# Kernel tuning notes

Hardware: AMD Instinct MI355X
Metric: run time of the kernel (lower is better)

The kernel has to match this reference:

```python
import jax, jax.numpy as jnp
import numpy as np

N_NODES = 50000
N_EDGES = 800000
D = 64
N_LAYERS = 3  # layer_dims = [64, 64, 64, 64]


def setup_inputs() -> dict:
    key = jax.random.key(0)
    ks = jax.random.split(key, 5)
    x = jax.random.normal(ks[0], (N_NODES, D), dtype=jnp.float32)
    edge_index = jax.random.randint(ks[1], (2, N_EDGES), 0, N_NODES, dtype=jnp.int64)
    scale = 1.0 / np.sqrt(D)
    # Per-layer restriction (message) maps, self-loop maps, and biases.
    W_msg = jax.random.normal(ks[2], (N_LAYERS, D, D), dtype=jnp.float32) * scale
    W_self = jax.random.normal(ks[3], (N_LAYERS, D, D), dtype=jnp.float32) * scale
    b = jax.random.normal(ks[4], (N_LAYERS, D), dtype=jnp.float32) * 0.01
    return {"x": x, "edge_index": edge_index, "W_msg": W_msg, "W_self": W_self, "b": b}


def reference(x, edge_index, W_msg, W_self, b):
    """Stacked sheaf conv layers: per-edge gather -> linear restriction ->
    scatter-sum aggregation to destination nodes + self-loop linear + bias,
    with ReLU between layers (none after the final layer)."""
    n = x.shape[0]
    src, dst = edge_index[0], edge_index[1]
    n_layers = W_msg.shape[0]
    for i in range(n_layers):
        msg = x[src] @ W_msg[i]                                   # [E, d] gather + restriction
        agg = jax.ops.segment_sum(msg, dst, num_segments=n)       # [N, d] scatter-add
        x = x @ W_self[i] + agg + b[i]                            # self-loop + aggregate + bias
        if i < n_layers - 1:
            x = jax.nn.relu(x)
    return x
```

## Files before the change

kernel.cpp:

```cpp
#include <hip/hip_runtime.h>

#define D 64

__device__ __forceinline__ unsigned short f2bf(float f) {
    unsigned u = __float_as_uint(f);
    unsigned r = (u + 0x7FFFu + ((u >> 16) & 1u)) >> 16;
    return (unsigned short)r;
}
__device__ __forceinline__ float bf2f(unsigned short h) {
    return __uint_as_float((unsigned)h << 16);
}

typedef __attribute__((ext_vector_type(8))) short bf16x8;
typedef __attribute__((ext_vector_type(4))) float f32x4;

__global__ void prep_kernel(const float* __restrict__ x, unsigned short* __restrict__ xb,
                            int total, int* __restrict__ deg, int N,
                            const float* __restrict__ Wself,
                            const float* __restrict__ Wmsg,
                            unsigned short* __restrict__ Bt, int n_layers) {
    int i = blockIdx.x * blockDim.x + threadIdx.x;
    if (i < N) deg[i] = 0;
    int wtotal = n_layers * D * 2 * D;
    if (i < wtotal) {
        int k = i & 127;
        int n = (i >> 7) & 63;
        int l = i >> 13;
        float w = (k < D) ? Wself[(size_t)l * D * D + k * D + n]
                          : Wmsg [(size_t)l * D * D + (k - D) * D + n];
        unsigned short hi = f2bf(w);
        unsigned short lo = f2bf(w - bf2f(hi));
        size_t base = (size_t)l * 2 * D * 2 * D;
        Bt[base + (size_t)n * 128 + k] = hi;
        Bt[base + 8192 + (size_t)n * 128 + k] = lo;
    }
    int base = i * 4;
    if (base + 4 <= total) {
        float4 v = *reinterpret_cast<const float4*>(x + base);
        ushort4 o;
        o.x = f2bf(v.x); o.y = f2bf(v.y); o.z = f2bf(v.z); o.w = f2bf(v.w);
        *reinterpret_cast<ushort4*>(xb + base) = o;
    } else if (base < total) {
        for (int k = base; k < total; ++k) xb[k] = f2bf(x[k]);
    }
}

__global__ void hist_rank_kernel(const int* __restrict__ dst, int* __restrict__ deg,
                                 int* __restrict__ rank, int E) {
    int i = blockIdx.x * blockDim.x + threadIdx.x;
    int base = i * 8;
    if (base + 8 <= E) {
        int4 d0 = *reinterpret_cast<const int4*>(dst + base);
        int4 d1 = *reinterpret_cast<const int4*>(dst + base + 4);
        int4 r0, r1;
        r0.x = atomicAdd(&deg[d0.x], 1);
        r0.y = atomicAdd(&deg[d0.y], 1);
        r0.z = atomicAdd(&deg[d0.z], 1);
        r0.w = atomicAdd(&deg[d0.w], 1);
        r1.x = atomicAdd(&deg[d1.x], 1);
        r1.y = atomicAdd(&deg[d1.y], 1);
        r1.z = atomicAdd(&deg[d1.z], 1);
        r1.w = atomicAdd(&deg[d1.w], 1);
        *reinterpret_cast<int4*>(rank + base) = r0;
        *reinterpret_cast<int4*>(rank + base + 4) = r1;
    } else {
        for (int e = base; e < E; ++e) rank[e] = atomicAdd(&deg[dst[e]], 1);
    }
}

__global__ void scan_k1(const int* __restrict__ deg, int* __restrict__ bsum, int n) {
    __shared__ int sh[256];
    int t = threadIdx.x;
    int g = blockIdx.x * 256 + t;
    int v = (g < n) ? deg[g] : 0;
    sh[t] = v;
    __syncthreads();
    for (int off = 1; off < 256; off <<= 1) {
        int u = (t >= off) ? sh[t - off] : 0;
        __syncthreads();
        sh[t] += u;
        __syncthreads();
    }
    if (t == 255) bsum[blockIdx.x] = sh[255];
}

__global__ void scan_k2(const int* __restrict__ bsum, int* __restrict__ boff, int nb) {
    __shared__ int sh[1024];
    int t = threadIdx.x;
    int v = (t < nb) ? bsum[t] : 0;
    sh[t] = v;
    __syncthreads();
    for (int off = 1; off < 1024; off <<= 1) {
        int u = (t >= off) ? sh[t - off] : 0;
        __syncthreads();
        sh[t] += u;
        __syncthreads();
    }
    if (t < nb) boff[t] = sh[t] - v;
}

__global__ void scan_k3(const int* __restrict__ deg, const int* __restrict__ boff,
                        int* __restrict__ row_ptr, int n) {
    __shared__ int sh[256];
    int t = threadIdx.x;
    int g = blockIdx.x * 256 + t;
    int v = (g < n) ? deg[g] : 0;
    sh[t] = v;
    __syncthreads();
    for (int off = 1; off < 256; off <<= 1) {
        int u = (t >= off) ? sh[t - off] : 0;
        __syncthreads();
        sh[t] += u;
        __syncthreads();
    }
    if (g < n) {
        int excl = sh[t] - v + boff[blockIdx.x];
        row_ptr[g] = excl;
        if (g == n - 1) row_ptr[n] = excl + v;
    }
}

__global__ void perm_rank_kernel(const int* __restrict__ src, const int* __restrict__ dst,
                                 const int* __restrict__ rank, const int* __restrict__ row_ptr,
                                 int* __restrict__ sorted_src, int E) {
    int i = blockIdx.x * blockDim.x + threadIdx.x;
    int base = i * 8;
    if (base + 8 <= E) {
        int4 d0 = *reinterpret_cast<const int4*>(dst + base);
        int4 d1 = *reinterpret_cast<const int4*>(dst + base + 4);
        int4 s0 = *reinterpret_cast<const int4*>(src + base);
        int4 s1 = *reinterpret_cast<const int4*>(src + base + 4);
        int4 r0 = *reinterpret_cast<const int4*>(rank + base);
        int4 r1 = *reinterpret_cast<const int4*>(rank + base + 4);
        int p0 = row_ptr[d0.x] + r0.x;
        int p1 = row_ptr[d0.y] + r0.y;
        int p2 = row_ptr[d0.z] + r0.z;
        int p3 = row_ptr[d0.w] + r0.w;
        int p4 = row_ptr[d1.x] + r1.x;
        int p5 = row_ptr[d1.y] + r1.y;
        int p6 = row_ptr[d1.z] + r1.z;
        int p7 = row_ptr[d1.w] + r1.w;
        __builtin_nontemporal_store(s0.x, &sorted_src[p0]);
        __builtin_nontemporal_store(s0.y, &sorted_src[p1]);
        __builtin_nontemporal_store(s0.z, &sorted_src[p2]);
        __builtin_nontemporal_store(s0.w, &sorted_src[p3]);
        __builtin_nontemporal_store(s1.x, &sorted_src[p4]);
        __builtin_nontemporal_store(s1.y, &sorted_src[p5]);
        __builtin_nontemporal_store(s1.z, &sorted_src[p6]);
        __builtin_nontemporal_store(s1.w, &sorted_src[p7]);
    } else {
        for (int e = base; e < E; ++e)
            sorted_src[row_ptr[dst[e]] + rank[e]] = src[e];
    }
}

__device__ __forceinline__ void acc16(float* ac, uint4 u0, uint4 u1) {
    ac[0]  += __uint_as_float(u0.x << 16);
    ac[1]  += __uint_as_float(u0.x & 0xFFFF0000u);
    ac[2]  += __uint_as_float(u0.y << 16);
    ac[3]  += __uint_as_float(u0.y & 0xFFFF0000u);
    ac[4]  += __uint_as_float(u0.z << 16);
    ac[5]  += __uint_as_float(u0.z & 0xFFFF0000u);
    ac[6]  += __uint_as_float(u0.w << 16);
    ac[7]  += __uint_as_float(u0.w & 0xFFFF0000u);
    ac[8]  += __uint_as_float(u1.x << 16);
    ac[9]  += __uint_as_float(u1.x & 0xFFFF0000u);
    ac[10] += __uint_as_float(u1.y << 16);
    ac[11] += __uint_as_float(u1.y & 0xFFFF0000u);
    ac[12] += __uint_as_float(u1.z << 16);
    ac[13] += __uint_as_float(u1.z & 0xFFFF0000u);
    ac[14] += __uint_as_float(u1.w << 16);
    ac[15] += __uint_as_float(u1.w & 0xFFFF0000u);
}

__global__ void __launch_bounds__(256)
fused_layer(const unsigned short* __restrict__ xb,
            const int* __restrict__ row_ptr,
            const int* __restrict__ sorted_src,
            const unsigned short* __restrict__ Bt,
            const float* __restrict__ bias,
            float* __restrict__ out_f32,
            unsigned short* __restrict__ out_bf16,
            int n_nodes, int E, int last) {
    __shared__ float red[4][16][68];

    int lane = threadIdx.x & 63;
    int w    = threadIdx.x >> 6;
    int ln15 = lane & 15;
    int lhi  = lane >> 4;

    int node0 = blockIdx.x << 4;
    int node  = node0 + ln15;
    int ncl   = min(node, n_nodes - 1);
    int beg = row_ptr[ncl];
    int end = row_ptr[ncl + 1];
    if (node >= n_nodes) end = beg;
    int deg = end - beg;

    int md = deg;
    md = max(md, __shfl_xor(md, 1));
    md = max(md, __shfl_xor(md, 2));
    md = max(md, __shfl_xor(md, 4));
    md = max(md, __shfl_xor(md, 8));

    float ac[16];
#pragma unroll
    for (int t = 0; t < 16; ++t) ac[t] = 0.f;

    const int Em1 = E - 1;
    int p = w;
    for (; p + 4 < md; p += 8) {
        int cA = min(beg + p,     Em1);
        int cB = min(beg + p + 4, Em1);
        int sA = sorted_src[cA];
        int sB = sorted_src[cB];
        const unsigned short* rA = xb + (((size_t)(unsigned)sA) << 6) + (lhi << 3);
        const unsigned short* rB = xb + (((size_t)(unsigned)sB) << 6) + (lhi << 3);
        uint4 a0 = *reinterpret_cast<const uint4*>(rA);
        uint4 a1 = *reinterpret_cast<const uint4*>(rA + 32);
        uint4 b0 = *reinterpret_cast<const uint4*>(rB);
        uint4 b1 = *reinterpret_cast<const uint4*>(rB + 32);
        if (p < deg)     acc16(ac, a0, a1);
        if (p + 4 < deg) acc16(ac, b0, b1);
    }
    for (; p < md; p += 4) {
        int cA = min(beg + p, Em1);
        int sA = sorted_src[cA];
        const unsigned short* rA = xb + (((size_t)(unsigned)sA) << 6) + (lhi << 3);
        uint4 a0 = *reinterpret_cast<const uint4*>(rA);
        uint4 a1 = *reinterpret_cast<const uint4*>(rA + 32);
        if (p < deg) acc16(ac, a0, a1);
    }

    int f0 = lhi << 3;
    *reinterpret_cast<float4*>(&red[w][ln15][f0])      = make_float4(ac[0], ac[1], ac[2], ac[3]);
    *reinterpret_cast<float4*>(&red[w][ln15][f0 + 4])  = make_float4(ac[4], ac[5], ac[6], ac[7]);
    *reinterpret_cast<float4*>(&red[w][ln15][32 + f0]) = make_float4(ac[8], ac[9], ac[10], ac[11]);
    *reinterpret_cast<float4*>(&red[w][ln15][36 + f0]) = make_float4(ac[12], ac[13], ac[14], ac[15]);

    bf16x8 Bf[2][4];
    {
        const unsigned short* bp = Bt + ((size_t)(w * 16 + ln15)) * 128 + (lhi << 3);
#pragma unroll
        for (int pp = 0; pp < 2; ++pp)
#pragma unroll
            for (int kc = 0; kc < 4; ++kc)
                Bf[pp][kc] = *reinterpret_cast<const bf16x8*>(bp + pp * 8192 + kc * 32);
    }
    const unsigned short* xr = xb + (((size_t)(unsigned)ncl) << 6) + (lhi << 3);
    bf16x8 A0 = *reinterpret_cast<const bf16x8*>(xr);
    bf16x8 A1 = *reinterpret_cast<const bf16x8*>(xr + 32);
    float bb = bias[w * 16 + ln15];

    __syncthreads();

    float s[16];
#pragma unroll
    for (int t = 0; t < 16; ++t) s[t] = 0.f;
#pragma unroll
    for (int ww = 0; ww < 4; ++ww) {
        float4 r0 = *reinterpret_cast<const float4*>(&red[ww][ln15][f0]);
        float4 r1 = *reinterpret_cast<const float4*>(&red[ww][ln15][f0 + 4]);
        float4 r2 = *reinterpret_cast<const float4*>(&red[ww][ln15][32 + f0]);
        float4 r3 = *reinterpret_cast<const float4*>(&red[ww][ln15][36 + f0]);
        s[0]  += r0.x; s[1]  += r0.y; s[2]  += r0.z; s[3]  += r0.w;
        s[4]  += r1.x; s[5]  += r1.y; s[6]  += r1.z; s[7]  += r1.w;
        s[8]  += r2.x; s[9]  += r2.y; s[10] += r2.z; s[11] += r2.w;
        s[12] += r3.x; s[13] += r3.y; s[14] += r3.z; s[15] += r3.w;
    }
    bf16x8 A2, A3;
#pragma unroll
    for (int t = 0; t < 8; ++t) A2[t] = (short)f2bf(s[t]);
#pragma unroll
    for (int t = 0; t < 8; ++t) A3[t] = (short)f2bf(s[8 + t]);

    f32x4 c = {0.f, 0.f, 0.f, 0.f};
    c = __builtin_amdgcn_mfma_f32_16x16x32_bf16(A0, Bf[0][0], c, 0, 0, 0);
    c = __builtin_amdgcn_mfma_f32_16x16x32_bf16(A0, Bf[1][0], c, 0, 0, 0);
    c = __builtin_amdgcn_mfma_f32_16x16x32_bf16(A1, Bf[0][1], c, 0, 0, 0);
    c = __builtin_amdgcn_mfma_f32_16x16x32_bf16(A1, Bf[1][1], c, 0, 0, 0);
    c = __builtin_amdgcn_mfma_f32_16x16x32_bf16(A2, Bf[0][2], c, 0, 0, 0);
    c = __builtin_amdgcn_mfma_f32_16x16x32_bf16(A2, Bf[1][2], c, 0, 0, 0);
    c = __builtin_amdgcn_mfma_f32_16x16x32_bf16(A3, Bf[0][3], c, 0, 0, 0);
    c = __builtin_amdgcn_mfma_f32_16x16x32_bf16(A3, Bf[1][3], c, 0, 0, 0);

    int colo = w * 16 + ln15;
    if (last) {
#pragma unroll
        for (int r = 0; r < 4; ++r) {
            int nr = node0 + lhi * 4 + r;
            if (nr < n_nodes)
                out_f32[((size_t)(unsigned)nr << 6) + colo] = c[r] + bb;
        }
    } else {
#pragma unroll
        for (int r = 0; r < 4; ++r) {
            int nr = node0 + lhi * 4 + r;
            if (nr < n_nodes)
                out_bf16[((size_t)(unsigned)nr << 6) + colo] = f2bf(fmaxf(c[r] + bb, 0.f));
        }
    }
}

__global__ void scatter_kernel(const float* __restrict__ x,
                               const int* __restrict__ src,
                               const int* __restrict__ dst,
                               float* __restrict__ agg, int n_edges) {
    int e = blockIdx.x * (blockDim.x >> 6) + (threadIdx.x >> 6);
    int lane = threadIdx.x & 63;
    if (e >= n_edges) return;
    float v = x[(size_t)src[e] * D + lane];
    unsafeAtomicAdd(&agg[(size_t)dst[e] * D + lane], v);
}

__global__ void dense_kernel(const float* __restrict__ xin,
                             const float* __restrict__ agg,
                             const float* __restrict__ Wself,
                             const float* __restrict__ Wmsg,
                             const float* __restrict__ bias,
                             float* __restrict__ xout,
                             int n_nodes, int do_relu) {
    __shared__ float Ws[D * D];
    __shared__ float Wm[D * D];
    for (int i = threadIdx.x; i < D * D; i += blockDim.x) {
        Ws[i] = Wself[i];
        Wm[i] = Wmsg[i];
    }
    __syncthreads();
    int lane = threadIdx.x & 63;
    int wave = threadIdx.x >> 6;
    int wpb = blockDim.x >> 6;
    float bj = bias[lane];
    for (int n = blockIdx.x * wpb + wave; n < n_nodes; n += gridDim.x * wpb) {
        float xv = xin[(size_t)n * D + lane];
        float av = agg[(size_t)n * D + lane];
        float acc = bj;
#pragma unroll
        for (int k = 0; k < D; ++k) {
            acc += __shfl(xv, k, 64) * Ws[k * D + lane]
                 + __shfl(av, k, 64) * Wm[k * D + lane];
        }
        if (do_relu) acc = fmaxf(acc, 0.f);
        xout[(size_t)n * D + lane] = acc;
    }
}

extern "C" void kernel_launch(void* const* d_in, const int* in_sizes, int n_in,
                              void* d_out, int out_size, void* d_ws, size_t ws_size,
                              hipStream_t stream) {
    const float* x0    = (const float*)d_in[0];
    const int*   ei    = (const int*)d_in[1];
    const float* Wmsg  = (const float*)d_in[2];
    const float* Wself = (const float*)d_in[3];
    const float* bias  = (const float*)d_in[4];
    float* out = (float*)d_out;

    const int N = in_sizes[0] / D;
    const int E = in_sizes[1] / 2;
    const int n_layers = in_sizes[4] / D;

    const int* src = ei;
    const int* dst = ei + E;
    const size_t NB = (size_t)N * D * sizeof(float);

    const int NBB = (N + 255) / 256;
    const size_t BtB = (size_t)n_layers * 2 * D * 2 * D * 2;
    const size_t need = (size_t)N * D * 2
                      + (size_t)N * D * 2
                      + BtB
                      + (size_t)E * 4
                      + (size_t)E * 4
                      + (size_t)(N + 1) * 4
                      + (size_t)N * 4
                      + (size_t)NBB * 4 * 2 + 256;

    if (ws_size >= need && NBB <= 1024) {
        char* p = (char*)d_ws;
        unsigned short* Xb   = (unsigned short*)p;  p += (size_t)N * D * 2;
        unsigned short* Xb2  = (unsigned short*)p;  p += (size_t)N * D * 2;
        unsigned short* Bt   = (unsigned short*)p;  p += BtB;
        int* sorted_src      = (int*)p;             p += (size_t)E * 4;
        int* rank            = (int*)p;             p += (size_t)E * 4;
        int* row_ptr         = (int*)p;             p += (size_t)(N + 1) * 4;
        int* deg             = (int*)p;             p += (size_t)N * 4;
        int* bsum            = (int*)p;             p += (size_t)NBB * 4;
        int* boff            = (int*)p;

        {
            int total = N * D;
            int nthr = (total + 3) / 4;
            prep_kernel<<<(nthr + 255) / 256, 256, 0, stream>>>(
                x0, Xb, total, deg, N, Wself, Wmsg, Bt, n_layers);

            int threads = 256;
            int nthr8 = (E + 7) / 8;
            int blocks = (nthr8 + threads - 1) / threads;
            hist_rank_kernel<<<blocks, threads, 0, stream>>>(dst, deg, rank, E);
            scan_k1<<<NBB, 256, 0, stream>>>(deg, bsum, N);
            scan_k2<<<1, 1024, 0, stream>>>(bsum, boff, NBB);
            scan_k3<<<NBB, 256, 0, stream>>>(deg, boff, row_ptr, N);
            perm_rank_kernel<<<blocks, threads, 0, stream>>>(src, dst, rank, row_ptr,
                                                             sorted_src, E);
        }

        const int dtiles = (N + 15) >> 4;
        const unsigned short* in_b = Xb;
        unsigned short* out_b = Xb2;

        for (int layer = 0; layer < n_layers; ++layer) {
            fused_layer<<<dtiles, 256, 0, stream>>>(
                in_b, row_ptr, sorted_src,
                Bt + (size_t)layer * 2 * D * 2 * D,
                bias + (size_t)layer * D,
                out, out_b, N, E, (layer == n_layers - 1) ? 1 : 0);
            const unsigned short* t = in_b;
            in_b = out_b;
            out_b = (unsigned short*)t;
        }
    } else {
        float* agg = (float*)d_ws;
        const int EPB = 256 / 64;
        const int scatter_blocks = (E + EPB - 1) / EPB;
        for (int layer = 0; layer < n_layers; ++layer) {
            hipMemsetAsync(agg, 0, NB, stream);
            const float* xin = (layer == 0) ? x0 : out;
            scatter_kernel<<<scatter_blocks, 256, 0, stream>>>(xin, src, dst, agg, E);
            dense_kernel<<<1024, 256, 0, stream>>>(
                xin, agg,
                Wself + (size_t)layer * D * D,
                Wmsg  + (size_t)layer * D * D,
                bias  + (size_t)layer * D,
                out, N, (layer < n_layers - 1) ? 1 : 0);
        }
    }
}
```

Measured before the change: 255.1 us.

## Sort nodes by in-degree so each fused-layer tile holds similar-degree nodes

Builds a degree histogram during the scan, scans it in descending-degree order, and scatters node ids into a permutation with atomics. Each fused_layer tile then processes 16 nodes of similar degree, taken from this permutation, and writes results back to their original rows. The goal is to shrink the per-tile max-degree loop, so lanes of low-degree nodes stop idling while the 16-lane group waits for its highest-degree node. The cost is an extra launch, heavily contended atomics on a few histogram bins, and scattered self-row reads and output writes.

After: 484.3 us. 1.9x slower.

```diff
diff --git a/kernel.cpp b/kernel.cpp
--- a/kernel.cpp
+++ b/kernel.cpp
@@ -18,9 +18,11 @@
                             int total, int* __restrict__ deg, int N,
                             const float* __restrict__ Wself,
                             const float* __restrict__ Wmsg,
-                            unsigned short* __restrict__ Bt, int n_layers) {
+                            unsigned short* __restrict__ Bt, int n_layers,
+                            int* __restrict__ dhist) {
     int i = blockIdx.x * blockDim.x + threadIdx.x;
     if (i < N) deg[i] = 0;
+    if (i < 1024) dhist[i] = 0;
     int wtotal = n_layers * D * 2 * D;
     if (i < wtotal) {
         int k = i & 127;
@@ -68,11 +70,13 @@
     }
 }
 
-__global__ void scan_k1(const int* __restrict__ deg, int* __restrict__ bsum, int n) {
+__global__ void scan_k1(const int* __restrict__ deg, int* __restrict__ bsum, int n,
+                        int* __restrict__ dhist) {
     __shared__ int sh[256];
     int t = threadIdx.x;
     int g = blockIdx.x * 256 + t;
     int v = (g < n) ? deg[g] : 0;
+    if (g < n) atomicAdd(&dhist[min(v, 1023)], 1);
     sh[t] = v;
     __syncthreads();
     for (int off = 1; off < 256; off <<= 1) {
@@ -84,7 +88,8 @@
     if (t == 255) bsum[blockIdx.x] = sh[255];
 }
 
-__global__ void scan_k2(const int* __restrict__ bsum, int* __restrict__ boff, int nb) {
+__global__ void scan_k2(const int* __restrict__ bsum, int* __restrict__ boff, int nb,
+                        const int* __restrict__ dhist, int* __restrict__ dbase) {
     __shared__ int sh[1024];
     int t = threadIdx.x;
     int v = (t < nb) ? bsum[t] : 0;
@@ -97,6 +102,18 @@
         __syncthreads();
     }
     if (t < nb) boff[t] = sh[t] - v;
+    __syncthreads();
+    int rb = 1023 - t;
+    int dv = dhist[rb];
+    sh[t] = dv;
+    __syncthreads();
+    for (int off = 1; off < 1024; off <<= 1) {
+        int u = (t >= off) ? sh[t - off] : 0;
+        __syncthreads();
+        sh[t] += u;
+        __syncthreads();
+    }
+    dbase[rb] = sh[t] - dv;
 }
 
 __global__ void scan_k3(const int* __restrict__ deg, const int* __restrict__ boff,
@@ -117,6 +134,16 @@
         int excl = sh[t] - v + boff[blockIdx.x];
         row_ptr[g] = excl;
         if (g == n - 1) row_ptr[n] = excl + v;
+    }
+}
+
+__global__ void perm_nodes_kernel(const int* __restrict__ deg, int* __restrict__ dbase,
+                                  int* __restrict__ nperm, int N) {
+    int n = blockIdx.x * blockDim.x + threadIdx.x;
+    if (n < N) {
+        int b = min(deg[n], 1023);
+        int pos = atomicAdd(&dbase[b], 1);
+        nperm[pos] = n;
     }
 }
 
@@ -177,12 +204,14 @@
 fused_layer(const unsigned short* __restrict__ xb,
             const int* __restrict__ row_ptr,
             const int* __restrict__ sorted_src,
+            const int* __restrict__ nperm,
             const unsigned short* __restrict__ Bt,
             const float* __restrict__ bias,
             float* __restrict__ out_f32,
             unsigned short* __restrict__ out_bf16,
             int n_nodes, int E, int last) {
     __shared__ float red[4][16][68];
+    __shared__ int snode[16];
 
     int lane = threadIdx.x & 63;
     int w    = threadIdx.x >> 6;
@@ -190,11 +219,14 @@
     int lhi  = lane >> 4;
 
     int node0 = blockIdx.x << 4;
-    int node  = node0 + ln15;
-    int ncl   = min(node, n_nodes - 1);
-    int beg = row_ptr[ncl];
-    int end = row_ptr[ncl + 1];
-    if (node >= n_nodes) end = beg;
+    int slot  = node0 + ln15;
+    int scl   = min(slot, n_nodes - 1);
+    int node  = nperm[scl];
+    if (lane < 16) snode[lane] = node;
+
+    int beg = row_ptr[node];
+    int end = row_ptr[node + 1];
+    if (slot >= n_nodes) end = beg;
     int deg = end - beg;
 
     int md = deg;
@@ -247,7 +279,7 @@
             for (int kc = 0; kc < 4; ++kc)
                 Bf[pp][kc] = *reinterpret_cast<const bf16x8*>(bp + pp * 8192 + kc * 32);
     }
-    const unsigned short* xr = xb + (((size_t)(unsigned)ncl) << 6) + (lhi << 3);
+    const unsigned short* xr = xb + (((size_t)(unsigned)node) << 6) + (lhi << 3);
     bf16x8 A0 = *reinterpret_cast<const bf16x8*>(xr);
     bf16x8 A1 = *reinterpret_cast<const bf16x8*>(xr + 32);
     float bb = bias[w * 16 + ln15];
@@ -288,16 +320,20 @@
     if (last) {
 #pragma unroll
         for (int r = 0; r < 4; ++r) {
-            int nr = node0 + lhi * 4 + r;
-            if (nr < n_nodes)
+            int sl = lhi * 4 + r;
+            if (node0 + sl < n_nodes) {
+                int nr = snode[sl];
                 out_f32[((size_t)(unsigned)nr << 6) + colo] = c[r] + bb;
+            }
         }
     } else {
 #pragma unroll
         for (int r = 0; r < 4; ++r) {
-            int nr = node0 + lhi * 4 + r;
-            if (nr < n_nodes)
+            int sl = lhi * 4 + r;
+            if (node0 + sl < n_nodes) {
+                int nr = snode[sl];
                 out_bf16[((size_t)(unsigned)nr << 6) + colo] = f2bf(fmaxf(c[r] + bb, 0.f));
+            }
         }
     }
 }
@@ -372,6 +408,8 @@
                       + (size_t)E * 4
                       + (size_t)(N + 1) * 4
                       + (size_t)N * 4
+                      + (size_t)N * 4
+                      + 1024 * 4 * 2
                       + (size_t)NBB * 4 * 2 + 256;
 
     if (ws_size >= need && NBB <= 1024) {
@@ -383,6 +421,9 @@
         int* rank            = (int*)p;             p += (size_t)E * 4;
         int* row_ptr         = (int*)p;             p += (size_t)(N + 1) * 4;
         int* deg             = (int*)p;             p += (size_t)N * 4;
+        int* nperm           = (int*)p;             p += (size_t)N * 4;
+        int* dhist           = (int*)p;             p += 1024 * 4;
+        int* dbase           = (int*)p;             p += 1024 * 4;
         int* bsum            = (int*)p;             p += (size_t)NBB * 4;
         int* boff            = (int*)p;
 
@@ -390,15 +431,16 @@
             int total = N * D;
             int nthr = (total + 3) / 4;
             prep_kernel<<<(nthr + 255) / 256, 256, 0, stream>>>(
-                x0, Xb, total, deg, N, Wself, Wmsg, Bt, n_layers);
+                x0, Xb, total, deg, N, Wself, Wmsg, Bt, n_layers, dhist);
 
             int threads = 256;
             int nthr8 = (E + 7) / 8;
             int blocks = (nthr8 + threads - 1) / threads;
             hist_rank_kernel<<<blocks, threads, 0, stream>>>(dst, deg, rank, E);
-            scan_k1<<<NBB, 256, 0, stream>>>(deg, bsum, N);
-            scan_k2<<<1, 1024, 0, stream>>>(bsum, boff, NBB);
+            scan_k1<<<NBB, 256, 0, stream>>>(deg, bsum, N, dhist);
+            scan_k2<<<1, 1024, 0, stream>>>(bsum, boff, NBB, dhist, dbase);
             scan_k3<<<NBB, 256, 0, stream>>>(deg, boff, row_ptr, N);
+            perm_nodes_kernel<<<NBB, 256, 0, stream>>>(deg, dbase, nperm, N);
             perm_rank_kernel<<<blocks, threads, 0, stream>>>(src, dst, rank, row_ptr,
                                                              sorted_src, E);
         }
@@ -409,7 +451,7 @@
 
         for (int layer = 0; layer < n_layers; ++layer) {
             fused_layer<<<dtiles, 256, 0, stream>>>(
-                in_b, row_ptr, sorted_src,
+                in_b, row_ptr, sorted_src, nperm,
                 Bt + (size_t)layer * 2 * D * 2 * D,
                 bias + (size_t)layer * D,
                 out, out_b, N, E, (layer == n_layers - 1) ? 1 : 0);
```
